# Optimization experiments

Hardware: AMD Instinct MI355X
Metric: run time of the kernel (lower is better)

Reference implementation:

```python
import jax, jax.numpy as jnp
import numpy as np

N = 50000      # nodes (src = dst at both layers)
E = 800000     # edges per layer
T = 8          # time steps
C_IN = 16      # input channels
HID = 16       # conv1 out channels (hardcoded in SAGENet)
C_OUT = 32     # final out channels


def setup_inputs() -> dict:
    key = jax.random.key(0)
    ks = jax.random.split(key, 10)
    X = jax.random.normal(ks[0], (T, N, C_IN), dtype=jnp.float32)
    edge_index0 = jax.random.randint(ks[1], (2, E), 0, N, dtype=jnp.int32)
    edge_weight0 = jax.random.uniform(ks[2], (E,), dtype=jnp.float32)
    edge_index1 = jax.random.randint(ks[3], (2, E), 0, N, dtype=jnp.int32)
    edge_weight1 = jax.random.uniform(ks[4], (E,), dtype=jnp.float32)
    res_n_id0 = jnp.arange(N, dtype=jnp.int32)
    res_n_id1 = jnp.arange(N, dtype=jnp.int32)
    W1 = jax.random.normal(ks[5], (2 * C_IN, HID), dtype=jnp.float32) * 0.1
    b1 = jax.random.normal(ks[6], (HID,), dtype=jnp.float32) * 0.1
    W2 = jax.random.normal(ks[7], (2 * HID, C_OUT), dtype=jnp.float32) * 0.1
    b2 = jax.random.normal(ks[8], (C_OUT,), dtype=jnp.float32) * 0.1
    return {"X": X, "edge_index0": edge_index0, "edge_weight0": edge_weight0,
            "edge_index1": edge_index1, "edge_weight1": edge_weight1,
            "res_n_id0": res_n_id0, "res_n_id1": res_n_id1,
            "W1": W1, "b1": b1, "W2": W2, "b2": b2}


def sage_conv(x, edge_index, edge_weight, res_n_id, num_dst, W, b):
    # x: [N_src, T, C]; message = edge_weight * x[src]; mean-aggregate to dst;
    # concat residual x[res_n_id] then linear (old PyG SAGEConv, concat=True).
    src, dst = edge_index[0], edge_index[1]
    msg = x[src] * edge_weight[:, None, None]                      # [E, T, C]
    summed = jax.ops.segment_sum(msg, dst, num_segments=num_dst)   # [Nd, T, C]
    cnt = jax.ops.segment_sum(jnp.ones_like(edge_weight), dst, num_segments=num_dst)
    aggr = summed / jnp.maximum(cnt, 1.0)[:, None, None]
    h = jnp.concatenate([x[res_n_id], aggr], axis=-1)              # [Nd, T, 2C]
    return jnp.einsum('ntc,cd->ntd', h, W) + b


def reference(X, edge_index0, edge_weight0, edge_index1, edge_weight1,
              res_n_id0, res_n_id1, W1, b1, W2, b2):
    x = jnp.transpose(X, (1, 0, 2))                                # [N, T, C]
    x = jax.nn.leaky_relu(sage_conv(x, edge_index0, edge_weight0, res_n_id0, N, W1, b1), 0.01)
    x = jax.nn.leaky_relu(sage_conv(x, edge_index1, edge_weight1, res_n_id1, N, W2, b2), 0.01)
    return jnp.transpose(x, (1, 0, 2))                             # [T, N, C_out]
```

## Files before the change

### kernel.cpp

```cpp
#include <hip/hip_runtime.h>
#include <hip/hip_bf16.h>
#include <stdint.h>

static constexpr int Nn   = 50000;
static constexpr int Ee   = 800000;
static constexpr int Tt   = 8;
static constexpr int CIN  = 16;
static constexpr int HID  = 16;
static constexpr int COUT = 32;
static constexpr int TC   = Tt * CIN;
static constexpr int ROWD = TC / 2;

static constexpr int NB  = (2 * Nn + 255) / 256;
static constexpr int CAP = 16;

static constexpr int WBUF_FLOATS = 1584;

__device__ inline float bflo(uint32_t u) { return __uint_as_float(u << 16); }
__device__ inline float bfhi(uint32_t u) { return __uint_as_float(u & 0xffff0000u); }
__device__ inline unsigned short f2bf(float x) {
    __hip_bfloat16 h = __float2bfloat16(x);
    unsigned short u; __builtin_memcpy(&u, &h, 2); return u;
}
__device__ inline uint32_t bfpack(float a, float b) {
    return (uint32_t)f2bf(a) | ((uint32_t)f2bf(b) << 16);
}

__global__ void k_detect_stage(const unsigned short* __restrict__ x16, int nvals,
                               int* __restrict__ flag,
                               const void* W1, const void* b1,
                               const void* W2, const void* b2,
                               float* __restrict__ wbuf,
                               int* __restrict__ bucketCnt) {
    __shared__ int bad;
    if (threadIdx.x == 0) bad = 0;
    __syncthreads();
    for (int i = threadIdx.x; i < nvals; i += 256) {
        int ex = (x16[i] >> 7) & 0xFF;
        if (ex >= 0x8D) atomicOr(&bad, 1);
    }
    __syncthreads();
    int f = bad;
    if (threadIdx.x == 0) flag[0] = f;
    for (int i = threadIdx.x; i < NB; i += 256) bucketCnt[i] = 0;
    for (int i = threadIdx.x; i < WBUF_FLOATS; i += 256) {
        const void* src; int idx;
        if (i < 512)       { src = W1; idx = i; }
        else if (i < 528)  { src = b1; idx = i - 512; }
        else if (i < 1552) { src = W2; idx = i - 528; }
        else               { src = b2; idx = i - 1552; }
        wbuf[i] = f ? ((const float*)src)[idx]
                    : __bfloat162float(((const __hip_bfloat16*)src)[idx]);
    }
}


__global__ __launch_bounds__(256) void k_count(const int* __restrict__ ei0,
                                               const int* __restrict__ ei1,
                                               int* __restrict__ bucketCnt) {
    __shared__ int hist[NB];
    for (int i = threadIdx.x; i < NB; i += 256) hist[i] = 0;
    __syncthreads();
    int stride = gridDim.x * 256;
    for (int e = blockIdx.x * 256 + threadIdx.x; e < 2 * Ee; e += stride) {
        int g = (e < Ee) ? ei0[Ee + e] : (Nn + ei1[Ee + (e - Ee)]);
        atomicAdd(&hist[g >> 8], 1);
    }
    __syncthreads();
    for (int i = threadIdx.x; i < NB; i += 256)
        if (hist[i]) atomicAdd(&bucketCnt[i], hist[i]);
}

__global__ void k_bucketscan(const int* __restrict__ bucketCnt,
                             int* __restrict__ base, int* __restrict__ gcur) {
    __shared__ int tmp[512];
    int tid = threadIdx.x;
    int v = (tid < NB) ? bucketCnt[tid] : 0;
    tmp[tid] = v;
    __syncthreads();
    for (int ofs = 1; ofs < 512; ofs <<= 1) {
        int t = (tid >= ofs) ? tmp[tid - ofs] : 0;
        __syncthreads();
        tmp[tid] += t;
        __syncthreads();
    }
    if (tid < NB) { int b = tmp[tid] - v; base[tid] = b; gcur[tid] = b; }
    if (tid == 0) base[NB] = 2 * Ee;
}

__global__ __launch_bounds__(256) void k_bin(const int* __restrict__ flag,
        const int* __restrict__ ei0, const void* w0v,
        const int* __restrict__ ei1, const void* w1v,
        int* __restrict__ gcur, uint64_t* __restrict__ gout) {
    __shared__ uint64_t rows[NB][CAP];
    __shared__ int cnt[NB];
    int tid = threadIdx.x;
    for (int i = tid; i < NB; i += 256) cnt[i] = 0;
    __syncthreads();
    int f = flag[0];
    int tileStride = gridDim.x * 256;
    for (int base_e = blockIdx.x * 256; base_e < 2 * Ee; base_e += tileStride) {
        int e = base_e + tid;
        if (e < 2 * Ee) {
            int g; uint32_t src, wb;
            if (e < Ee) {
                g = ei0[Ee + e];
                src = (uint32_t)ei0[e];
                wb = f ? f2bf(((const float*)w0v)[e]) : ((const unsigned short*)w0v)[e];
            } else {
                int e1 = e - Ee;
                g = Nn + ei1[Ee + e1];
                src = (uint32_t)ei1[e1];
                wb = f ? f2bf(((const float*)w1v)[e1]) : ((const unsigned short*)w1v)[e1];
            }
            uint64_t r = ((uint64_t)(uint32_t)g << 32) | (src << 16) | wb;
            int b = g >> 8;
            int idx = atomicAdd(&cnt[b], 1);
            if (idx < CAP) rows[b][idx] = r;
            else { int pos = atomicAdd(&gcur[b], 1); gout[pos] = r; }
        }
        __syncthreads();
        for (int b = tid; b < NB; b += 256) {
            if (cnt[b] >= CAP) {
                int pos = atomicAdd(&gcur[b], CAP);
#pragma unroll
                for (int k = 0; k < CAP; k++) gout[pos + k] = rows[b][k];
                cnt[b] = 0;
            }
        }
        __syncthreads();
    }
    for (int b = tid; b < NB; b += 256) {
        int c = cnt[b];
        if (c > 0) {
            int pos = atomicAdd(&gcur[b], c);
            for (int k = 0; k < c; k++) gout[pos + k] = rows[b][k];
        }
    }
}

__global__ __launch_bounds__(256) void k_csr(const int* __restrict__ base,
        const uint64_t* __restrict__ gout,
        int* __restrict__ off, uint32_t* __restrict__ rec) {
    __shared__ int hist[256];
    __shared__ int tmp[256];
    __shared__ int cur[256];
    int b = blockIdx.x, tid = threadIdx.x;
    int lo = base[b], hi = base[b + 1];
    hist[tid] = 0;
    __syncthreads();
    for (int i = lo + tid; i < hi; i += 256) {
        int gl = (int)(gout[i] >> 32) & 255;
        atomicAdd(&hist[gl], 1);
    }
    __syncthreads();
    int v = hist[tid];
    tmp[tid] = v;
    __syncthreads();
    for (int ofs = 1; ofs < 256; ofs <<= 1) {
        int t = (tid >= ofs) ? tmp[tid - ofs] : 0;
        __syncthreads();
        tmp[tid] += t;
        __syncthreads();
    }
    int excl = tmp[tid] - v;
    int gg = (b << 8) + tid;
    if (gg < 2 * Nn) off[gg] = lo + excl;
    if (b == NB - 1 && tid == 0) off[2 * Nn] = 2 * Ee;
    cur[tid] = lo + excl;
    __syncthreads();
    for (int i = lo + tid; i < hi; i += 256) {
        uint64_t r = gout[i];
        int gl = (int)(r >> 32) & 255;
        int pos = atomicAdd(&cur[gl], 1);
        rec[pos] = (uint32_t)r;
    }
}

__global__ void k_transpose(const int* __restrict__ flag, const void* Xv,
                            uint32_t* __restrict__ xrows) {
    int f = flag[0];
    int i = blockIdx.x * blockDim.x + threadIdx.x;
    if (i >= Nn * ROWD) return;
    int n = i >> 6;
    int l = i & 63;
    int t = l >> 3;
    int c = (l & 7) * 2;
    int sidx = (t * Nn + n) * CIN + c;
    uint32_t v;
    if (f) {
        float2 ab = ((const float2*)Xv)[sidx >> 1];
        v = bfpack(ab.x, ab.y);
    } else {
        const unsigned short* u = (const unsigned short*)Xv;
        v = (uint32_t)u[sidx] | ((uint32_t)u[sidx + 1] << 16);
    }
    xrows[i] = v;
}


__global__ __launch_bounds__(256) void k_layer1(
    const uint32_t* __restrict__ xrows, const int* __restrict__ off,
    const uint32_t* __restrict__ rec, const int* __restrict__ resid,
    const float* __restrict__ wbuf, uint32_t* __restrict__ h1rows) {
    __shared__ float Ws[32 * 16];
    __shared__ float bs[16];
    __shared__ float sh[4][256];
    int tid = threadIdx.x;
    int wv = tid >> 6, lane = tid & 63;
    for (int i = tid; i < 512; i += 256) Ws[i] = wbuf[i];
    if (tid < 16) bs[tid] = wbuf[512 + tid];
    int n = blockIdx.x * 4 + wv;
    int o0 = __builtin_amdgcn_readfirstlane(off[n]);
    int o1 = __builtin_amdgcn_readfirstlane(off[n + 1]);
    int rn = __builtin_amdgcn_readfirstlane(resid[n]);
    uint32_t xv = xrows[rn * ROWD + lane];
    float alo = 0.f, ahi = 0.f;
    int j = o0;
    for (; j + 4 <= o1; j += 4) {
        uint32_t e0 = rec[j], e1 = rec[j + 1], e2 = rec[j + 2], e3 = rec[j + 3];
        uint32_t g0 = xrows[(e0 >> 16) * ROWD + lane];
        uint32_t g1 = xrows[(e1 >> 16) * ROWD + lane];
        uint32_t g2 = xrows[(e2 >> 16) * ROWD + lane];
        uint32_t g3 = xrows[(e3 >> 16) * ROWD + lane];
        float w0 = bflo(e0), w1 = bflo(e1), w2 = bflo(e2), w3 = bflo(e3);
        alo += w0 * bflo(g0) + w1 * bflo(g1) + w2 * bflo(g2) + w3 * bflo(g3);
        ahi += w0 * bfhi(g0) + w1 * bfhi(g1) + w2 * bfhi(g2) + w3 * bfhi(g3);
    }
    for (; j < o1; j++) {
        uint32_t e0 = rec[j];
        uint32_t g0 = xrows[(e0 >> 16) * ROWD + lane];
        float w0 = bflo(e0);
        alo += w0 * bflo(g0);
        ahi += w0 * bfhi(g0);
    }
    float inv = 1.f / (float)max(o1 - o0, 1);
    float* xs = &sh[wv][0];
    float* ag = &sh[wv][128];
    xs[2 * lane] = bflo(xv);
    xs[2 * lane + 1] = bfhi(xv);
    ag[2 * lane] = alo * inv;
    ag[2 * lane + 1] = ahi * inv;
    __syncthreads();
    int t = lane >> 3;
    int c0 = (2 * lane) & 15;
    const float* xr = &xs[t * 16];
    const float* ar = &ag[t * 16];
    float v0 = bs[c0], v1 = bs[c0 + 1];
#pragma unroll
    for (int k = 0; k < 16; k++) {
        float xk = xr[k], ak = ar[k];
        v0 += xk * Ws[k * 16 + c0] + ak * Ws[(16 + k) * 16 + c0];
        v1 += xk * Ws[k * 16 + c0 + 1] + ak * Ws[(16 + k) * 16 + c0 + 1];
    }
    v0 = v0 > 0.f ? v0 : 0.01f * v0;
    v1 = v1 > 0.f ? v1 : 0.01f * v1;
    h1rows[n * ROWD + lane] = bfpack(v0, v1);
}

__global__ __launch_bounds__(256) void k_layer2(
    const int* __restrict__ flag,
    const uint32_t* __restrict__ h1rows, const int* __restrict__ off,
    const uint32_t* __restrict__ rec, const int* __restrict__ resid,
    const float* __restrict__ wbuf, void* __restrict__ outv) {
    __shared__ float Ws[32 * 32];
    __shared__ float bs[32];
    __shared__ float sh[4][256];
    int tid = threadIdx.x;
    int wv = tid >> 6, lane = tid & 63;
    for (int i = tid; i < 1024; i += 256) Ws[i] = wbuf[528 + i];
    if (tid < 32) bs[tid] = wbuf[1552 + tid];
    int f = flag[0];
    int n = blockIdx.x * 4 + wv;
    int o0 = __builtin_amdgcn_readfirstlane(off[Nn + n]);
    int o1 = __builtin_amdgcn_readfirstlane(off[Nn + n + 1]);
    int rn = __builtin_amdgcn_readfirstlane(resid[n]);
    uint32_t xv = h1rows[rn * ROWD + lane];
    float alo = 0.f, ahi = 0.f;
    int j = o0;
    for (; j + 4 <= o1; j += 4) {
        uint32_t e0 = rec[j], e1 = rec[j + 1], e2 = rec[j + 2], e3 = rec[j + 3];
        uint32_t g0 = h1rows[(e0 >> 16) * ROWD + lane];
        uint32_t g1 = h1rows[(e1 >> 16) * ROWD + lane];
        uint32_t g2 = h1rows[(e2 >> 16) * ROWD + lane];
        uint32_t g3 = h1rows[(e3 >> 16) * ROWD + lane];
        float w0 = bflo(e0), w1 = bflo(e1), w2 = bflo(e2), w3 = bflo(e3);
        alo += w0 * bflo(g0) + w1 * bflo(g1) + w2 * bflo(g2) + w3 * bflo(g3);
        ahi += w0 * bfhi(g0) + w1 * bfhi(g1) + w2 * bfhi(g2) + w3 * bfhi(g3);
    }
    for (; j < o1; j++) {
        uint32_t e0 = rec[j];
        uint32_t g0 = h1rows[(e0 >> 16) * ROWD + lane];
        float w0 = bflo(e0);
        alo += w0 * bflo(g0);
        ahi += w0 * bfhi(g0);
    }
    float inv = 1.f / (float)max(o1 - o0, 1);
    float* xs = &sh[wv][0];
    float* ag = &sh[wv][128];
    xs[2 * lane] = bflo(xv);
    xs[2 * lane + 1] = bfhi(xv);
    ag[2 * lane] = alo * inv;
    ag[2 * lane + 1] = ahi * inv;
    __syncthreads();
    int h = lane & 31;
    int tb = lane >> 5;
#pragma unroll
    for (int q = 0; q < 4; q++) {
        int t = tb + 2 * q;
        const float* xr = &xs[t * 16];
        const float* ar = &ag[t * 16];
        float v = bs[h];
#pragma unroll
        for (int k = 0; k < 16; k++) {
            v += xr[k] * Ws[k * 32 + h] + ar[k] * Ws[(16 + k) * 32 + h];
        }
        v = v > 0.f ? v : 0.01f * v;
        size_t idx = ((size_t)(t * Nn + n)) * COUT + h;
        if (f) ((float*)outv)[idx] = v;
        else   ((__hip_bfloat16*)outv)[idx] = __float2bfloat16(v);
    }
}


extern "C" void kernel_launch(void* const* d_in, const int* in_sizes, int n_in,
                              void* d_out, int out_size, void* d_ws, size_t ws_size,
                              hipStream_t stream) {
    const void* X   = d_in[0];
    const int* ei0  = (const int*)d_in[1];
    const void* w0  = d_in[2];
    const int* ei1  = (const int*)d_in[3];
    const void* w1  = d_in[4];
    const int* rn0  = (const int*)d_in[5];
    const int* rn1  = (const int*)d_in[6];
    const void* W1  = d_in[7];
    const void* b1  = d_in[8];
    const void* W2  = d_in[9];
    const void* b2  = d_in[10];

    char* ws = (char*)d_ws;
    size_t p = 0;
    auto alloc = [&](size_t bytes) -> char* {
        p = (p + 255) & ~(size_t)255;
        char* r = ws + p;
        p += bytes;
        return r;
    };
    int* flag       = (int*)alloc(4);
    float* wbuf     = (float*)alloc(WBUF_FLOATS * 4);
    int* bucketCnt  = (int*)alloc(NB * 4);
    int* base       = (int*)alloc((NB + 1) * 4);
    int* gcur       = (int*)alloc(NB * 4);
    int* off        = (int*)alloc(((size_t)2 * Nn + 1) * 4);
    uint32_t* recf  = (uint32_t*)alloc((size_t)2 * Ee * 4);
    uint32_t* h1rows= (uint32_t*)alloc((size_t)Nn * ROWD * 4);
    uint64_t* gout  = (uint64_t*)alloc((size_t)2 * Ee * 8);
    uint32_t* xrows = (uint32_t*)gout;

    hipLaunchKernelGGL(k_detect_stage, dim3(1), dim3(256), 0, stream,
                       (const unsigned short*)X, 16384, flag, W1, b1, W2, b2,
                       wbuf, bucketCnt);
    hipLaunchKernelGGL(k_count, dim3(256), dim3(256), 0, stream,
                       ei0, ei1, bucketCnt);
    hipLaunchKernelGGL(k_bucketscan, dim3(1), dim3(512), 0, stream,
                       bucketCnt, base, gcur);
    hipLaunchKernelGGL(k_bin, dim3(512), dim3(256), 0, stream,
                       flag, ei0, w0, ei1, w1, gcur, gout);
    hipLaunchKernelGGL(k_csr, dim3(NB), dim3(256), 0, stream,
                       base, gout, off, recf);
    hipLaunchKernelGGL(k_transpose, dim3((Nn * ROWD + 255) / 256), dim3(256), 0, stream,
                       flag, X, xrows);
    hipLaunchKernelGGL(k_layer1, dim3(Nn / 4), dim3(256), 0, stream,
                       xrows, off, recf, rn0, wbuf, h1rows);
    hipLaunchKernelGGL(k_layer2, dim3(Nn / 4), dim3(256), 0, stream,
                       flag, h1rows, off, recf, rn1, wbuf, d_out);
    (void)in_sizes; (void)n_in; (void)out_size; (void)ws_size;
}
```

Baseline: 282.4 us.

## Vectorize edge counting, stage CSR scatter in LDS, deepen gather unroll

The bucket histogram kernel now reads destination indices as int4 vectors. The CSR build first scatters records into a shared-memory staging buffer and then writes them out contiguously, so global writes are coalesced when a bucket fits. Both layer kernels unroll the neighbor gather by 8 with loads issued before the arithmetic, which raises memory-level parallelism. The block barrier moves from after the per-wave aggregation to right after the weight load, relying on each wave reading only its own shared slice. The 32 KB staging array raises LDS use in the CSR kernel, and the per-wave reads now assume wave-synchronous LDS visibility.

```diff
diff --git a/kernel.cpp b/kernel.cpp
--- a/kernel.cpp
+++ b/kernel.cpp
@@ -61,10 +61,18 @@
     __shared__ int hist[NB];
     for (int i = threadIdx.x; i < NB; i += 256) hist[i] = 0;
     __syncthreads();
+    const int4* d0 = (const int4*)(ei0 + Ee);
+    const int4* d1 = (const int4*)(ei1 + Ee);
     int stride = gridDim.x * 256;
-    for (int e = blockIdx.x * 256 + threadIdx.x; e < 2 * Ee; e += stride) {
-        int g = (e < Ee) ? ei0[Ee + e] : (Nn + ei1[Ee + (e - Ee)]);
-        atomicAdd(&hist[g >> 8], 1);
+    int nq = Ee / 4;
+    for (int i = blockIdx.x * 256 + threadIdx.x; i < 2 * nq; i += stride) {
+        int4 v; int addn;
+        if (i < nq) { v = d0[i]; addn = 0; }
+        else        { v = d1[i - nq]; addn = Nn; }
+        atomicAdd(&hist[(v.x + addn) >> 8], 1);
+        atomicAdd(&hist[(v.y + addn) >> 8], 1);
+        atomicAdd(&hist[(v.z + addn) >> 8], 1);
+        atomicAdd(&hist[(v.w + addn) >> 8], 1);
     }
     __syncthreads();
     for (int i = threadIdx.x; i < NB; i += 256)
@@ -145,6 +153,7 @@
     __shared__ int hist[256];
     __shared__ int tmp[256];
     __shared__ int cur[256];
+    __shared__ uint32_t stage[8192];
     int b = blockIdx.x, tid = threadIdx.x;
     int lo = base[b], hi = base[b + 1];
     hist[tid] = 0;
@@ -167,13 +176,27 @@
     int gg = (b << 8) + tid;
     if (gg < 2 * Nn) off[gg] = lo + excl;
     if (b == NB - 1 && tid == 0) off[2 * Nn] = 2 * Ee;
-    cur[tid] = lo + excl;
-    __syncthreads();
-    for (int i = lo + tid; i < hi; i += 256) {
-        uint64_t r = gout[i];
-        int gl = (int)(r >> 32) & 255;
-        int pos = atomicAdd(&cur[gl], 1);
-        rec[pos] = (uint32_t)r;
+    int count = hi - lo;
+    if (count <= 8192) {
+        cur[tid] = excl;
+        __syncthreads();
+        for (int i = lo + tid; i < hi; i += 256) {
+            uint64_t r = gout[i];
+            int gl = (int)(r >> 32) & 255;
+            int pos = atomicAdd(&cur[gl], 1);
+            stage[pos] = (uint32_t)r;
+        }
+        __syncthreads();
+        for (int i = tid; i < count; i += 256) rec[lo + i] = stage[i];
+    } else {
+        cur[tid] = lo + excl;
+        __syncthreads();
+        for (int i = lo + tid; i < hi; i += 256) {
+            uint64_t r = gout[i];
+            int gl = (int)(r >> 32) & 255;
+            int pos = atomicAdd(&cur[gl], 1);
+            rec[pos] = (uint32_t)r;
+        }
     }
 }
 
@@ -210,6 +233,7 @@
     int wv = tid >> 6, lane = tid & 63;
     for (int i = tid; i < 512; i += 256) Ws[i] = wbuf[i];
     if (tid < 16) bs[tid] = wbuf[512 + tid];
+    __syncthreads();
     int n = blockIdx.x * 4 + wv;
     int o0 = __builtin_amdgcn_readfirstlane(off[n]);
     int o1 = __builtin_amdgcn_readfirstlane(off[n + 1]);
@@ -217,15 +241,18 @@
     uint32_t xv = xrows[rn * ROWD + lane];
     float alo = 0.f, ahi = 0.f;
     int j = o0;
-    for (; j + 4 <= o1; j += 4) {
-        uint32_t e0 = rec[j], e1 = rec[j + 1], e2 = rec[j + 2], e3 = rec[j + 3];
-        uint32_t g0 = xrows[(e0 >> 16) * ROWD + lane];
-        uint32_t g1 = xrows[(e1 >> 16) * ROWD + lane];
-        uint32_t g2 = xrows[(e2 >> 16) * ROWD + lane];
-        uint32_t g3 = xrows[(e3 >> 16) * ROWD + lane];
-        float w0 = bflo(e0), w1 = bflo(e1), w2 = bflo(e2), w3 = bflo(e3);
-        alo += w0 * bflo(g0) + w1 * bflo(g1) + w2 * bflo(g2) + w3 * bflo(g3);
-        ahi += w0 * bfhi(g0) + w1 * bfhi(g1) + w2 * bfhi(g2) + w3 * bfhi(g3);
+    for (; j + 8 <= o1; j += 8) {
+        uint32_t e[8], g[8];
+#pragma unroll
+        for (int k = 0; k < 8; k++) e[k] = rec[j + k];
+#pragma unroll
+        for (int k = 0; k < 8; k++) g[k] = xrows[(e[k] >> 16) * ROWD + lane];
+#pragma unroll
+        for (int k = 0; k < 8; k++) {
+            float w = bflo(e[k]);
+            alo += w * bflo(g[k]);
+            ahi += w * bfhi(g[k]);
+        }
     }
     for (; j < o1; j++) {
         uint32_t e0 = rec[j];
@@ -241,7 +268,6 @@
     xs[2 * lane + 1] = bfhi(xv);
     ag[2 * lane] = alo * inv;
     ag[2 * lane + 1] = ahi * inv;
-    __syncthreads();
     int t = lane >> 3;
     int c0 = (2 * lane) & 15;
     const float* xr = &xs[t * 16];
@@ -270,6 +296,7 @@
     int wv = tid >> 6, lane = tid & 63;
     for (int i = tid; i < 1024; i += 256) Ws[i] = wbuf[528 + i];
     if (tid < 32) bs[tid] = wbuf[1552 + tid];
+    __syncthreads();
     int f = flag[0];
     int n = blockIdx.x * 4 + wv;
     int o0 = __builtin_amdgcn_readfirstlane(off[Nn + n]);
@@ -278,15 +305,18 @@
     uint32_t xv = h1rows[rn * ROWD + lane];
     float alo = 0.f, ahi = 0.f;
     int j = o0;
-    for (; j + 4 <= o1; j += 4) {
-        uint32_t e0 = rec[j], e1 = rec[j + 1], e2 = rec[j + 2], e3 = rec[j + 3];
-        uint32_t g0 = h1rows[(e0 >> 16) * ROWD + lane];
-        uint32_t g1 = h1rows[(e1 >> 16) * ROWD + lane];
-        uint32_t g2 = h1rows[(e2 >> 16) * ROWD + lane];
-        uint32_t g3 = h1rows[(e3 >> 16) * ROWD + lane];
-        float w0 = bflo(e0), w1 = bflo(e1), w2 = bflo(e2), w3 = bflo(e3);
-        alo += w0 * bflo(g0) + w1 * bflo(g1) + w2 * bflo(g2) + w3 * bflo(g3);
-        ahi += w0 * bfhi(g0) + w1 * bfhi(g1) + w2 * bfhi(g2) + w3 * bfhi(g3);
+    for (; j + 8 <= o1; j += 8) {
+        uint32_t e[8], g[8];
+#pragma unroll
+        for (int k = 0; k < 8; k++) e[k] = rec[j + k];
+#pragma unroll
+        for (int k = 0; k < 8; k++) g[k] = h1rows[(e[k] >> 16) * ROWD + lane];
+#pragma unroll
+        for (int k = 0; k < 8; k++) {
+            float w = bflo(e[k]);
+            alo += w * bflo(g[k]);
+            ahi += w * bfhi(g[k]);
+        }
     }
     for (; j < o1; j++) {
         uint32_t e0 = rec[j];
@@ -302,7 +332,6 @@
     xs[2 * lane + 1] = bfhi(xv);
     ag[2 * lane] = alo * inv;
     ag[2 * lane + 1] = ahi * inv;
-    __syncthreads();
     int h = lane & 31;
     int tb = lane >> 5;
 #pragma unroll
```

Result: faster. 276.3 us (-2.2%).
